# Kernel optimization log

Hardware: AMD Instinct MI355X
Metric: run time of the kernel (lower is better)

Reference implementation:

```python
import math
import jax, jax.numpy as jnp
import numpy as np


def _pairwise_sqdist(x, y):
    # x: [N, d], y: [M, d] -> [N, M]
    x2 = jnp.sum(x * x, axis=-1)[:, None]
    y2 = jnp.sum(y * y, axis=-1)[None, :]
    return jnp.maximum(x2 + y2 - 2.0 * (x @ y.T), 0.0)


def setup_inputs() -> dict:
    key = jax.random.key(0)
    k1, k2 = jax.random.split(key)
    N, M, D = 8192, 8192, 2
    base_points = jax.random.normal(k1, (N, D), dtype=jnp.float32)
    target_points = jax.random.normal(k2, (M, D), dtype=jnp.float32)
    log_sigma = jnp.asarray(math.log(0.1), dtype=jnp.float32)
    log_scale = jnp.zeros((D,), dtype=jnp.float32)
    return {
        "base_points": base_points,
        "target_points": target_points,
        "log_sigma": log_sigma,
        "log_scale": log_scale,
    }


def reference(base_points, target_points, log_sigma, log_scale):
    # learn_scale=True: anisotropic per-coordinate scaling
    scale = jnp.exp(log_scale)
    base = base_points * scale
    target = target_points * scale

    # uniform node weights (use_weight_net=False)
    N = base.shape[0]
    M = target.shape[0]
    w_base = jnp.full((N,), 1.0 / N, dtype=base.dtype)
    w_target = jnp.full((M,), 1.0 / M, dtype=target.dtype)

    # center=True: subtract weighted centroid of each cloud
    base = base - jnp.sum(w_base[:, None] * base, axis=0, keepdims=True)
    target = target - jnp.sum(w_target[:, None] * target, axis=0, keepdims=True)

    sigma = jnp.exp(log_sigma)
    inv2s2 = 1.0 / (2.0 * sigma * sigma)

    k_bb = jnp.exp(-_pairwise_sqdist(base, base) * inv2s2)      # [N, N]
    k_tt = jnp.exp(-_pairwise_sqdist(target, target) * inv2s2)  # [M, M]
    k_bt = jnp.exp(-_pairwise_sqdist(base, target) * inv2s2)    # [N, M]

    term_bb = w_base @ (k_bb @ w_base)
    term_tt = w_target @ (k_tt @ w_target)
    term_bt = w_base @ (k_bt @ w_target)
    loss = term_bb + term_tt - 2.0 * term_bt
    return loss
```

## Files before the change

kernel.cpp:

```cpp
#include <hip/hip_runtime.h>


#define BLOCK    256
#define NT_CROSS 1024
#define NT_TOT   3072
#define NBUCK    512
#define BXMIN    (-64.0f)
#define BSCALE   4.0f
#define CUT      5.2915026f
#define LOG2E    1.4426950408889634f

typedef float v2f __attribute__((ext_vector_type(2)));

__device__ __forceinline__ float fexp2(float x) {
    return __builtin_amdgcn_exp2f(x);
}

__global__ __launch_bounds__(1024) void sort_kernel(
    const float* __restrict__ base, const float* __restrict__ target,
    const float* __restrict__ log_sigma, const float* __restrict__ log_scale,
    int N, int M,
    float* __restrict__ xsB, float* __restrict__ ysB, float* __restrict__ csB,
    float* __restrict__ xsT, float* __restrict__ ysT, float* __restrict__ csT,
    double* __restrict__ msum, double* __restrict__ slots)
{
    __shared__ unsigned hist[NBUCK], pref[NBUCK], cnt[NBUCK];
    __shared__ double mred[16][2];
    const int tid = threadIdx.x;
    const bool isB = (blockIdx.x == 0);
    if (isB && tid < 64) slots[tid] = 0.0;

    const float sigma = expf(log_sigma[0]);
    const float sq = sqrtf((0.5f / (sigma * sigma)) * LOG2E);
    const float f0 = expf(log_scale[0]) * sq;
    const float f1 = expf(log_scale[1]) * sq;

    const float2* src = (const float2*)(isB ? base : target);
    const int n = isB ? N : M;
    float* xs = isB ? xsB : xsT;
    float* ys = isB ? ysB : ysT;
    float* cs = isB ? csB : csT;

    for (int i = tid; i < NBUCK; i += 1024) { hist[i] = 0u; cnt[i] = 0u; }
    __syncthreads();

    double sx = 0.0, sy = 0.0;
    for (int i = tid; i < n; i += 1024) {
        float2 a = src[i];
        float x = a.x * f0, y = a.y * f1;
        sx += (double)x; sy += (double)y;
        int b = min(max((int)((x - BXMIN) * BSCALE), 0), NBUCK - 1);
        atomicAdd(&hist[b], 1u);
    }
    for (int off = 32; off; off >>= 1) {
        sx += __shfl_down(sx, off);
        sy += __shfl_down(sy, off);
    }
    if ((tid & 63) == 0) { mred[tid >> 6][0] = sx; mred[tid >> 6][1] = sy; }
    __syncthreads();
    if (tid == 0) {
        double ax = 0, ay = 0;
        for (int k = 0; k < 16; ++k) { ax += mred[k][0]; ay += mred[k][1]; }
        msum[2 * blockIdx.x] = ax; msum[2 * blockIdx.x + 1] = ay;
    }

    if (tid < NBUCK) pref[tid] = hist[tid];
    __syncthreads();
    for (int off = 1; off < NBUCK; off <<= 1) {
        unsigned v = 0u;
        if (tid < NBUCK && tid >= off) v = pref[tid - off];
        __syncthreads();
        if (tid < NBUCK) pref[tid] += v;
        __syncthreads();
    }
    for (int i = tid; i < n; i += 1024) {
        float2 a = src[i];
        float x = a.x * f0, y = a.y * f1;
        int b = min(max((int)((x - BXMIN) * BSCALE), 0), NBUCK - 1);
        unsigned pos = pref[b] - hist[b] + atomicAdd(&cnt[b], 1u);
        xs[pos] = x;
        ys[pos] = y;
        cs[pos] = -fmaf(x, x, y * y);
    }
}

__global__ __launch_bounds__(BLOCK, 8) void mmd_main(
    int N, int M,
    const float* __restrict__ xsB, const float* __restrict__ ysB,
    const float* __restrict__ csB,
    const float* __restrict__ xsT, const float* __restrict__ ysT,
    const float* __restrict__ csT,
    const double* __restrict__ msum, double* __restrict__ slots)
{
    __shared__ __align__(16) float tbx[256];
    __shared__ __align__(16) float tby[256];
    __shared__ __align__(16) float tbc[256];
    __shared__ __align__(8)  float2 qb[64];
    __shared__ double wredd[4];

    const int tid = threadIdx.x;
    const int t   = blockIdx.x;

    const double wNN = 1.0 / ((double)N * (double)N);
    const double wMM = 1.0 / ((double)M * (double)M);
    const double wNM = -2.0 / ((double)N * (double)M);

    int rt, phase, term;
    bool sym;
    const float *xA, *yA, *xB, *yB, *cB;
    double wt;
    float shx = 0.f, shy = 0.f;
    if (t < NT_CROSS) {
        sym = false; term = 2;
        rt = t >> 5; phase = t & 31;
        xA = xsB; yA = ysB; xB = xsT; yB = ysT; cB = csT;
        wt = wNM;
        shx = (float)(msum[0] / (double)N - msum[2] / (double)M);
        shy = (float)(msum[1] / (double)N - msum[3] / (double)M);
    } else {
        sym = true;
        const int u = t - NT_CROSS;
        term = (u >= 1024) ? 1 : 0;
        const int v = u & 1023;
        rt = v >> 5; phase = v & 31;
        if (term) { xA = xsT; yA = ysT; xB = xsT; yB = ysT; cB = csT; }
        else      { xA = xsB; yA = ysB; xB = xsB; yB = ysB; cB = csB; }
        wt = 2.0 * (term ? wMM : wNN);
    }
    const int i0  = rt * 256;
    const int jq0 = 4 * phase;

    {
        const int g = tid & 63;
        const int addr = jq0 + 128 * g;
        if (tid < 64) {
            float4 v4 = *(const float4*)(xB + addr);
            *(float4*)&tbx[4 * g] = v4;
            qb[g] = make_float2(fminf(fminf(v4.x, v4.y), fminf(v4.z, v4.w)),
                                fmaxf(fmaxf(v4.x, v4.y), fmaxf(v4.z, v4.w)));
        } else if (tid < 128) {
            *(float4*)&tby[4 * g] = *(const float4*)(yB + addr);
        } else if (tid < 192) {
            *(float4*)&tbc[4 * g] = *(const float4*)(cB + addr);
        }
    }
    __syncthreads();

    const int u_    = tid & 127;
    const int r0    = i0 + 2 * u_;
    const int qoff  = (tid >> 7) * 32;
    const int wr_lo = i0 + ((tid >> 6) & 1) * 128;
    const int wr_hi = wr_lo + 127;

    float2 xr = *(const float2*)(xA + r0);
    float2 yr = *(const float2*)(yA + r0);
    const float axr0 = xr.x - shx, axr1 = xr.y - shx;
    const float ayr0 = yr.x - shy, ayr1 = yr.y - shy;
    const float ax2s[2] = { axr0 + axr0, axr1 + axr1 };
    const float ay2s[2] = { ayr0 + ayr0, ayr1 + ayr1 };
    const float A0s[2]  = { -fmaf(axr0, axr0, ayr0 * ayr0),
                            -fmaf(axr1, axr1, ayr1 * ayr1) };

    float rmin = fminf(axr0, axr1), rmax = fmaxf(axr0, axr1);
    for (int off = 32; off; off >>= 1) {
        rmin = fminf(rmin, __shfl_xor(rmin, off));
        rmax = fmaxf(rmax, __shfl_xor(rmax, off));
    }
    const float rminc = rmin - CUT, rmaxc = rmax + CUT;

    v2f s00 = {0.f, 0.f}, s01 = {0.f, 0.f};
    v2f s10 = {0.f, 0.f}, s11 = {0.f, 0.f};
    float sge = 0.f, sgt = 0.f;

    if (!sym) {
#pragma unroll 2
        for (int m = 0; m < 32; ++m) {
            const int qi = qoff + m;
            float2 qr = qb[qi];
            if (qr.x > rmaxc || qr.y < rminc) continue;
            float4 BX = *(const float4*)&tbx[4 * qi];
            float4 BY = *(const float4*)&tby[4 * qi];
            float4 C  = *(const float4*)&tbc[4 * qi];
            v2f bxa = { BX.x, BX.y }, bxb = { BX.z, BX.w };
            v2f bya = { BY.x, BY.y }, byb = { BY.z, BY.w };
            v2f ca  = { C.x,  C.y  }, cb  = { C.z,  C.w  };
            {
                v2f A0v = { A0s[0], A0s[0] };
                v2f axv = { ax2s[0], ax2s[0] };
                v2f ayv = { ay2s[0], ay2s[0] };
                v2f ea = axv * bxa + (ayv * bya + (ca + A0v));
                v2f eb = axv * bxb + (ayv * byb + (cb + A0v));
                s00 += (v2f){ fexp2(ea.x), fexp2(ea.y) };
                s01 += (v2f){ fexp2(eb.x), fexp2(eb.y) };
            }
            {
                v2f A0v = { A0s[1], A0s[1] };
                v2f axv = { ax2s[1], ax2s[1] };
                v2f ayv = { ay2s[1], ay2s[1] };
                v2f ea = axv * bxa + (ayv * bya + (ca + A0v));
                v2f eb = axv * bxb + (ayv * byb + (cb + A0v));
                s10 += (v2f){ fexp2(ea.x), fexp2(ea.y) };
                s11 += (v2f){ fexp2(eb.x), fexp2(eb.y) };
            }
        }
    } else {
#pragma unroll 2
        for (int m = 0; m < 32; ++m) {
            const int qi = qoff + m;
            const int jq = jq0 + 128 * qi;
            if (jq + 3 < wr_lo) continue;
            const bool mask = (jq <= wr_hi);
            float2 qr = qb[qi];
            if (!mask && (qr.x > rmaxc || qr.y < rminc)) continue;
            float4 BX = *(const float4*)&tbx[4 * qi];
            float4 BY = *(const float4*)&tby[4 * qi];
            float4 C  = *(const float4*)&tbc[4 * qi];
            if (!mask) {
                v2f bxa = { BX.x, BX.y }, bxb = { BX.z, BX.w };
                v2f bya = { BY.x, BY.y }, byb = { BY.z, BY.w };
                v2f ca  = { C.x,  C.y  }, cb  = { C.z,  C.w  };
                {
                    v2f A0v = { A0s[0], A0s[0] };
                    v2f axv = { ax2s[0], ax2s[0] };
                    v2f ayv = { ay2s[0], ay2s[0] };
                    v2f ea = axv * bxa + (ayv * bya + (ca + A0v));
                    v2f eb = axv * bxb + (ayv * byb + (cb + A0v));
                    s00 += (v2f){ fexp2(ea.x), fexp2(ea.y) };
                    s01 += (v2f){ fexp2(eb.x), fexp2(eb.y) };
                }
                {
                    v2f A0v = { A0s[1], A0s[1] };
                    v2f axv = { ax2s[1], ax2s[1] };
                    v2f ayv = { ay2s[1], ay2s[1] };
                    v2f ea = axv * bxa + (ayv * bya + (ca + A0v));
                    v2f eb = axv * bxb + (ayv * byb + (cb + A0v));
                    s10 += (v2f){ fexp2(ea.x), fexp2(ea.y) };
                    s11 += (v2f){ fexp2(eb.x), fexp2(eb.y) };
                }
            } else {
#pragma unroll
                for (int k = 0; k < 2; ++k) {
                    const int row = r0 + k;
                    float e0 = fmaf(ax2s[k], BX.x, fmaf(ay2s[k], BY.x, C.x + A0s[k]));
                    float e1 = fmaf(ax2s[k], BX.y, fmaf(ay2s[k], BY.y, C.y + A0s[k]));
                    float e2 = fmaf(ax2s[k], BX.z, fmaf(ay2s[k], BY.z, C.z + A0s[k]));
                    float e3 = fmaf(ax2s[k], BX.w, fmaf(ay2s[k], BY.w, C.w + A0s[k]));
                    float v0 = fexp2(e0), v1 = fexp2(e1);
                    float v2 = fexp2(e2), v3 = fexp2(e3);
                    sge += (jq + 0 >= row) ? v0 : 0.f;  sgt += (jq + 0 > row) ? v0 : 0.f;
                    sge += (jq + 1 >= row) ? v1 : 0.f;  sgt += (jq + 1 > row) ? v1 : 0.f;
                    sge += (jq + 2 >= row) ? v2 : 0.f;  sgt += (jq + 2 > row) ? v2 : 0.f;
                    sge += (jq + 3 >= row) ? v3 : 0.f;  sgt += (jq + 3 > row) ? v3 : 0.f;
                }
            }
        }
    }

    v2f st0 = s00 + s01, st1 = s10 + s11;
    double result = wt * ((double)(st0.x + st0.y) + (double)(st1.x + st1.y));
    if (sym) result += (term ? wMM : wNN) * (double)(sge + sgt);

    for (int off = 32; off; off >>= 1) result += __shfl_down(result, off);
    if ((tid & 63) == 0) wredd[tid >> 6] = result;
    __syncthreads();
    if (tid == 0) {
        double s = wredd[0] + wredd[1] + wredd[2] + wredd[3];
        atomicAdd(&slots[t & 63], s);
    }
}

__global__ void final_kernel(const double* __restrict__ slots,
                             float* __restrict__ out)
{
    const int tid = threadIdx.x;
    double s = slots[tid];
    for (int off = 32; off; off >>= 1) s += __shfl_down(s, off);
    if (tid == 0) out[0] = (float)s;
}

extern "C" void kernel_launch(void* const* d_in, const int* in_sizes, int n_in,
                              void* d_out, int out_size, void* d_ws, size_t ws_size,
                              hipStream_t stream)
{
    const float* base      = (const float*)d_in[0];
    const float* target    = (const float*)d_in[1];
    const float* log_sigma = (const float*)d_in[2];
    const float* log_scale = (const float*)d_in[3];
    float* out = (float*)d_out;

    int N = in_sizes[0] / 2;
    int M = in_sizes[1] / 2;

    char* ws = (char*)d_ws;
    double* msum  = (double*)ws;
    double* slots = (double*)(ws + 64);
    float*  arr   = (float*)(ws + 1024);
    float* xsB = arr;
    float* ysB = xsB + N;
    float* csB = ysB + N;
    float* xsT = csB + N;
    float* ysT = xsT + M;
    float* csT = ysT + M;

    sort_kernel<<<2, 1024, 0, stream>>>(base, target, log_sigma, log_scale,
                                        N, M, xsB, ysB, csB, xsT, ysT, csT,
                                        msum, slots);
    mmd_main<<<NT_TOT, BLOCK, 0, stream>>>(N, M, xsB, ysB, csB,
                                           xsT, ysT, csT, msum, slots);
    final_kernel<<<1, 64, 0, stream>>>(slots, out);
}
```

Before: 98.92 us.

## Tighten cutoff, ballot-driven tile skipping, wave-scan prefix, fuse final reduction

Shrinks the Gaussian cutoff radius so more distant tiles are skipped. The per-row loop is replaced by a wave-wide ballot that builds masks of surviving tiles and iterates only over set bits. The histogram prefix sum becomes a single-wave shuffle scan, launch bounds are relaxed to allow more registers, and the separate final kernel is replaced by a last-block-done counter inside the main kernel. The smaller cutoff drops more kernel tail mass, which may shift accuracy, and the last-block pattern relies on threadfence ordering.

```diff
diff --git a/kernel.cpp b/kernel.cpp
--- a/kernel.cpp
+++ b/kernel.cpp
@@ -7,7 +7,7 @@
 #define NBUCK    512
 #define BXMIN    (-64.0f)
 #define BSCALE   4.0f
-#define CUT      5.2915026f
+#define CUT      4.8989795f
 #define LOG2E    1.4426950408889634f
 
 typedef float v2f __attribute__((ext_vector_type(2)));
@@ -22,13 +22,17 @@
     int N, int M,
     float* __restrict__ xsB, float* __restrict__ ysB, float* __restrict__ csB,
     float* __restrict__ xsT, float* __restrict__ ysT, float* __restrict__ csT,
-    double* __restrict__ msum, double* __restrict__ slots)
+    double* __restrict__ msum, double* __restrict__ slots,
+    unsigned* __restrict__ dctr)
 {
     __shared__ unsigned hist[NBUCK], pref[NBUCK], cnt[NBUCK];
     __shared__ double mred[16][2];
     const int tid = threadIdx.x;
     const bool isB = (blockIdx.x == 0);
-    if (isB && tid < 64) slots[tid] = 0.0;
+    if (isB) {
+        if (tid < 64) slots[tid] = 0.0;
+        if (tid == 64) *dctr = 0u;
+    }
 
     const float sigma = expf(log_sigma[0]);
     const float sq = sqrtf((0.5f / (sigma * sigma)) * LOG2E);
@@ -64,39 +68,49 @@
         msum[2 * blockIdx.x] = ax; msum[2 * blockIdx.x + 1] = ay;
     }
 
-    if (tid < NBUCK) pref[tid] = hist[tid];
-    __syncthreads();
-    for (int off = 1; off < NBUCK; off <<= 1) {
-        unsigned v = 0u;
-        if (tid < NBUCK && tid >= off) v = pref[tid - off];
-        __syncthreads();
-        if (tid < NBUCK) pref[tid] += v;
-        __syncthreads();
-    }
+    if (tid < 64) {
+        unsigned loc[8], run = 0;
+        const int b0 = tid * 8;
+#pragma unroll
+        for (int k = 0; k < 8; ++k) { loc[k] = run; run += hist[b0 + k]; }
+        const unsigned tot = run;
+        unsigned pre = tot;
+        for (int off = 1; off < 64; off <<= 1) {
+            unsigned nbr = __shfl_up(pre, off);
+            if (tid >= off) pre += nbr;
+        }
+        pre -= tot;
+#pragma unroll
+        for (int k = 0; k < 8; ++k) pref[b0 + k] = pre + loc[k];
+    }
+    __syncthreads();
+
     for (int i = tid; i < n; i += 1024) {
         float2 a = src[i];
         float x = a.x * f0, y = a.y * f1;
         int b = min(max((int)((x - BXMIN) * BSCALE), 0), NBUCK - 1);
-        unsigned pos = pref[b] - hist[b] + atomicAdd(&cnt[b], 1u);
+        unsigned pos = pref[b] + atomicAdd(&cnt[b], 1u);
         xs[pos] = x;
         ys[pos] = y;
         cs[pos] = -fmaf(x, x, y * y);
     }
 }
 
-__global__ __launch_bounds__(BLOCK, 8) void mmd_main(
+__global__ __launch_bounds__(BLOCK, 4) void mmd_main(
     int N, int M,
     const float* __restrict__ xsB, const float* __restrict__ ysB,
     const float* __restrict__ csB,
     const float* __restrict__ xsT, const float* __restrict__ ysT,
     const float* __restrict__ csT,
-    const double* __restrict__ msum, double* __restrict__ slots)
+    const double* __restrict__ msum, double* __restrict__ slots,
+    unsigned* __restrict__ dctr, float* __restrict__ out)
 {
     __shared__ __align__(16) float tbx[256];
     __shared__ __align__(16) float tby[256];
     __shared__ __align__(16) float tbc[256];
     __shared__ __align__(8)  float2 qb[64];
     __shared__ double wredd[4];
+    __shared__ int lastf;
 
     const int tid = threadIdx.x;
     const int t   = blockIdx.x;
@@ -168,91 +182,77 @@
     }
     const float rminc = rmin - CUT, rmaxc = rmax + CUT;
 
+    const int lm   = tid & 31;
+    const int qlm  = qoff + lm;
+    float2 qrm = qb[qlm];
+    const bool xs_ok = !(qrm.x > rmaxc || qrm.y < rminc);
+    unsigned fmask, bmask = 0u;
+    if (!sym) {
+        fmask = (unsigned)__ballot(xs_ok);
+    } else {
+        const int jqm = jq0 + 128 * qlm;
+        const bool below = (jqm + 3) < wr_lo;
+        const bool band  = !below && (jqm <= wr_hi);
+        const bool fullq = !below && !band && xs_ok;
+        fmask = (unsigned)__ballot(fullq);
+        bmask = (unsigned)__ballot(band);
+    }
+
     v2f s00 = {0.f, 0.f}, s01 = {0.f, 0.f};
     v2f s10 = {0.f, 0.f}, s11 = {0.f, 0.f};
+
+    while (fmask) {
+        const int m = __builtin_ctz(fmask);
+        fmask &= fmask - 1;
+        const int qi = qoff + m;
+        float4 BX = *(const float4*)&tbx[4 * qi];
+        float4 BY = *(const float4*)&tby[4 * qi];
+        float4 C  = *(const float4*)&tbc[4 * qi];
+        v2f bxa = { BX.x, BX.y }, bxb = { BX.z, BX.w };
+        v2f bya = { BY.x, BY.y }, byb = { BY.z, BY.w };
+        v2f ca  = { C.x,  C.y  }, cb  = { C.z,  C.w  };
+        {
+            v2f A0v = { A0s[0], A0s[0] };
+            v2f axv = { ax2s[0], ax2s[0] };
+            v2f ayv = { ay2s[0], ay2s[0] };
+            v2f ea = axv * bxa + (ayv * bya + (ca + A0v));
+            v2f eb = axv * bxb + (ayv * byb + (cb + A0v));
+            s00 += (v2f){ fexp2(ea.x), fexp2(ea.y) };
+            s01 += (v2f){ fexp2(eb.x), fexp2(eb.y) };
+        }
+        {
+            v2f A0v = { A0s[1], A0s[1] };
+            v2f axv = { ax2s[1], ax2s[1] };
+            v2f ayv = { ay2s[1], ay2s[1] };
+            v2f ea = axv * bxa + (ayv * bya + (ca + A0v));
+            v2f eb = axv * bxb + (ayv * byb + (cb + A0v));
+            s10 += (v2f){ fexp2(ea.x), fexp2(ea.y) };
+            s11 += (v2f){ fexp2(eb.x), fexp2(eb.y) };
+        }
+    }
+
     float sge = 0.f, sgt = 0.f;
-
-    if (!sym) {
-#pragma unroll 2
-        for (int m = 0; m < 32; ++m) {
-            const int qi = qoff + m;
-            float2 qr = qb[qi];
-            if (qr.x > rmaxc || qr.y < rminc) continue;
-            float4 BX = *(const float4*)&tbx[4 * qi];
-            float4 BY = *(const float4*)&tby[4 * qi];
-            float4 C  = *(const float4*)&tbc[4 * qi];
-            v2f bxa = { BX.x, BX.y }, bxb = { BX.z, BX.w };
-            v2f bya = { BY.x, BY.y }, byb = { BY.z, BY.w };
-            v2f ca  = { C.x,  C.y  }, cb  = { C.z,  C.w  };
-            {
-                v2f A0v = { A0s[0], A0s[0] };
-                v2f axv = { ax2s[0], ax2s[0] };
-                v2f ayv = { ay2s[0], ay2s[0] };
-                v2f ea = axv * bxa + (ayv * bya + (ca + A0v));
-                v2f eb = axv * bxb + (ayv * byb + (cb + A0v));
-                s00 += (v2f){ fexp2(ea.x), fexp2(ea.y) };
-                s01 += (v2f){ fexp2(eb.x), fexp2(eb.y) };
-            }
-            {
-                v2f A0v = { A0s[1], A0s[1] };
-                v2f axv = { ax2s[1], ax2s[1] };
-                v2f ayv = { ay2s[1], ay2s[1] };
-                v2f ea = axv * bxa + (ayv * bya + (ca + A0v));
-                v2f eb = axv * bxb + (ayv * byb + (cb + A0v));
-                s10 += (v2f){ fexp2(ea.x), fexp2(ea.y) };
-                s11 += (v2f){ fexp2(eb.x), fexp2(eb.y) };
-            }
-        }
-    } else {
-#pragma unroll 2
-        for (int m = 0; m < 32; ++m) {
-            const int qi = qoff + m;
-            const int jq = jq0 + 128 * qi;
-            if (jq + 3 < wr_lo) continue;
-            const bool mask = (jq <= wr_hi);
-            float2 qr = qb[qi];
-            if (!mask && (qr.x > rmaxc || qr.y < rminc)) continue;
-            float4 BX = *(const float4*)&tbx[4 * qi];
-            float4 BY = *(const float4*)&tby[4 * qi];
-            float4 C  = *(const float4*)&tbc[4 * qi];
-            if (!mask) {
-                v2f bxa = { BX.x, BX.y }, bxb = { BX.z, BX.w };
-                v2f bya = { BY.x, BY.y }, byb = { BY.z, BY.w };
-                v2f ca  = { C.x,  C.y  }, cb  = { C.z,  C.w  };
-                {
-                    v2f A0v = { A0s[0], A0s[0] };
-                    v2f axv = { ax2s[0], ax2s[0] };
-                    v2f ayv = { ay2s[0], ay2s[0] };
-                    v2f ea = axv * bxa + (ayv * bya + (ca + A0v));
-                    v2f eb = axv * bxb + (ayv * byb + (cb + A0v));
-                    s00 += (v2f){ fexp2(ea.x), fexp2(ea.y) };
-                    s01 += (v2f){ fexp2(eb.x), fexp2(eb.y) };
-                }
-                {
-                    v2f A0v = { A0s[1], A0s[1] };
-                    v2f axv = { ax2s[1], ax2s[1] };
-                    v2f ayv = { ay2s[1], ay2s[1] };
-                    v2f ea = axv * bxa + (ayv * bya + (ca + A0v));
-                    v2f eb = axv * bxb + (ayv * byb + (cb + A0v));
-                    s10 += (v2f){ fexp2(ea.x), fexp2(ea.y) };
-                    s11 += (v2f){ fexp2(eb.x), fexp2(eb.y) };
-                }
-            } else {
+    while (bmask) {
+        const int m = __builtin_ctz(bmask);
+        bmask &= bmask - 1;
+        const int qi = qoff + m;
+        const int jq = jq0 + 128 * qi;
+        float4 BX = *(const float4*)&tbx[4 * qi];
+        float4 BY = *(const float4*)&tby[4 * qi];
+        float4 C  = *(const float4*)&tbc[4 * qi];
 #pragma unroll
-                for (int k = 0; k < 2; ++k) {
-                    const int row = r0 + k;
-                    float e0 = fmaf(ax2s[k], BX.x, fmaf(ay2s[k], BY.x, C.x + A0s[k]));
-                    float e1 = fmaf(ax2s[k], BX.y, fmaf(ay2s[k], BY.y, C.y + A0s[k]));
-                    float e2 = fmaf(ax2s[k], BX.z, fmaf(ay2s[k], BY.z, C.z + A0s[k]));
-                    float e3 = fmaf(ax2s[k], BX.w, fmaf(ay2s[k], BY.w, C.w + A0s[k]));
-                    float v0 = fexp2(e0), v1 = fexp2(e1);
-                    float v2 = fexp2(e2), v3 = fexp2(e3);
-                    sge += (jq + 0 >= row) ? v0 : 0.f;  sgt += (jq + 0 > row) ? v0 : 0.f;
-                    sge += (jq + 1 >= row) ? v1 : 0.f;  sgt += (jq + 1 > row) ? v1 : 0.f;
-                    sge += (jq + 2 >= row) ? v2 : 0.f;  sgt += (jq + 2 > row) ? v2 : 0.f;
-                    sge += (jq + 3 >= row) ? v3 : 0.f;  sgt += (jq + 3 > row) ? v3 : 0.f;
-                }
-            }
+        for (int k = 0; k < 2; ++k) {
+            const int row = r0 + k;
+            float e0 = fmaf(ax2s[k], BX.x, fmaf(ay2s[k], BY.x, C.x + A0s[k]));
+            float e1 = fmaf(ax2s[k], BX.y, fmaf(ay2s[k], BY.y, C.y + A0s[k]));
+            float e2 = fmaf(ax2s[k], BX.z, fmaf(ay2s[k], BY.z, C.z + A0s[k]));
+            float e3 = fmaf(ax2s[k], BX.w, fmaf(ay2s[k], BY.w, C.w + A0s[k]));
+            float v0 = fexp2(e0), v1 = fexp2(e1);
+            float v2 = fexp2(e2), v3 = fexp2(e3);
+            sge += (jq + 0 >= row) ? v0 : 0.f;  sgt += (jq + 0 > row) ? v0 : 0.f;
+            sge += (jq + 1 >= row) ? v1 : 0.f;  sgt += (jq + 1 > row) ? v1 : 0.f;
+            sge += (jq + 2 >= row) ? v2 : 0.f;  sgt += (jq + 2 > row) ? v2 : 0.f;
+            sge += (jq + 3 >= row) ? v3 : 0.f;  sgt += (jq + 3 > row) ? v3 : 0.f;
         }
     }
 
@@ -266,16 +266,20 @@
     if (tid == 0) {
         double s = wredd[0] + wredd[1] + wredd[2] + wredd[3];
         atomicAdd(&slots[t & 63], s);
-    }
-}
-
-__global__ void final_kernel(const double* __restrict__ slots,
-                             float* __restrict__ out)
-{
-    const int tid = threadIdx.x;
-    double s = slots[tid];
-    for (int off = 32; off; off >>= 1) s += __shfl_down(s, off);
-    if (tid == 0) out[0] = (float)s;
+        __threadfence();
+        unsigned d = atomicAdd(dctr, 1u);
+        lastf = (d == (unsigned)(NT_TOT - 1)) ? 1 : 0;
+    }
+    __syncthreads();
+    if (lastf) {
+        __threadfence();
+        double v = 0.0;
+        if (tid < 64) v = atomicAdd(&slots[tid], 0.0);
+        if (tid < 64) {
+            for (int off = 32; off; off >>= 1) v += __shfl_down(v, off);
+            if (tid == 0) out[0] = (float)v;
+        }
+    }
 }
 
 extern "C" void kernel_launch(void* const* d_in, const int* in_sizes, int n_in,
@@ -292,9 +296,10 @@
     int M = in_sizes[1] / 2;
 
     char* ws = (char*)d_ws;
-    double* msum  = (double*)ws;
-    double* slots = (double*)(ws + 64);
-    float*  arr   = (float*)(ws + 1024);
+    double*   msum  = (double*)ws;
+    double*   slots = (double*)(ws + 64);
+    unsigned* dctr  = (unsigned*)(ws + 640);
+    float*    arr   = (float*)(ws + 1024);
     float* xsB = arr;
     float* ysB = xsB + N;
     float* csB = ysB + N;
@@ -304,8 +309,8 @@
 
     sort_kernel<<<2, 1024, 0, stream>>>(base, target, log_sigma, log_scale,
                                         N, M, xsB, ysB, csB, xsT, ysT, csT,
-                                        msum, slots);
+                                        msum, slots, dctr);
     mmd_main<<<NT_TOT, BLOCK, 0, stream>>>(N, M, xsB, ysB, csB,
-                                           xsT, ysT, csT, msum, slots);
-    final_kernel<<<1, 64, 0, stream>>>(slots, out);
+                                           xsT, ysT, csT, msum, slots,
+                                           dctr, out);
 }
```

After: 131.3 us. 1.33x slower.
